# Optimization experiments

Hardware: AMD Instinct MI355X
Metric: run time of the kernel (lower is better)

Reference implementation:

```python
import jax, jax.numpy as jnp
import numpy as np

B, D_S, D_E, D_K, D_C, D_P, D_W, D_M, N_MEM, N_LEV = 2048, 1024, 1024, 256, 1024, 1024, 512, 1024, 4096, 3
SAT = 10.0


def _ln(x, scale, bias, eps=1e-6):
    mu = jnp.mean(x, axis=-1, keepdims=True)
    var = jnp.var(x, axis=-1, keepdims=True)
    return (x - mu) * jax.lax.rsqrt(var + eps) * scale + bias


def setup_inputs() -> dict:
    key = jax.random.key(0)
    ks = iter(jax.random.split(key, 48))
    rn = lambda shape, s=0.02: jax.random.normal(next(ks), shape, dtype=jnp.float32) * s
    h_q = D_S + D_E
    h_p = D_P + D_C
    return {
        "s_prev": rn((B, D_S), 1.0), "w_prev": rn((B, D_W), 1.0),
        "p_prev": rn((B, D_P), 1.0), "e_t": rn((B, D_E), 1.0),
        "M0": rn((N_MEM, D_M), 1.0), "M1": rn((N_MEM, D_M), 1.0), "M2": rn((N_MEM, D_M), 1.0),
        "K0": rn((N_MEM, D_K), 1.0), "K1": rn((N_MEM, D_K), 1.0), "K2": rn((N_MEM, D_K), 1.0),
        "Wq1": rn((h_q, h_q)), "bq1": jnp.zeros((h_q,), jnp.float32),
        "ln_q_scale": jnp.ones((h_q,), jnp.float32), "ln_q_bias": jnp.zeros((h_q,), jnp.float32),
        "Wq2": rn((h_q, D_K)), "bq2": jnp.zeros((D_K,), jnp.float32),
        "Wl0": rn((D_M, D_C)), "Wl1": rn((D_M, D_C)), "Wl2": rn((D_M, D_C)),
        "Wmix": rn((N_LEV * D_C, N_LEV)), "bmix": jnp.zeros((N_LEV,), jnp.float32),
        "Wz": rn((D_E, D_P)), "bz": jnp.zeros((D_P,), jnp.float32),
        "A_diag": jnp.zeros((D_W,), jnp.float32),
        "A_U": rn((D_W, D_W // 4), 0.01), "A_V": rn((D_W, D_W // 4), 0.01),
        "Wamod": rn((D_C, D_W)), "bamod": jnp.zeros((D_W,), jnp.float32),
        "WB": rn((D_C + D_P, D_W)), "bB": jnp.zeros((D_W,), jnp.float32),
        "Wp1": rn((h_p, h_p)), "bp1": jnp.zeros((h_p,), jnp.float32),
        "ln_p_scale": jnp.ones((h_p,), jnp.float32), "ln_p_bias": jnp.zeros((h_p,), jnp.float32),
        "Wp2": rn((h_p, D_P)), "bp2": jnp.zeros((D_P,), jnp.float32),
        "Wg": rn((D_S + D_E + D_C, D_S)), "bg": jnp.zeros((D_S,), jnp.float32),
        "U_p": rn((D_S, D_P)), "U_w": rn((D_S, D_W)),
    }


def _cell(s_prev, w_prev, p_prev, e_t, Ms, Ks, Wls,
          Wq1, bq1, ln_q_scale, ln_q_bias, Wq2, bq2, Wmix, bmix,
          Wz, bz, A_diag, A_U, A_V, Wamod, bamod, WB, bB,
          Wp1, bp1, ln_p_scale, ln_p_bias, Wp2, bp2, Wg, bg, U_p, U_w):
    # ---- CMS read: query -> per-level softmax attention -> mixed context ----
    q = jax.nn.relu(_ln(jnp.concatenate([s_prev, e_t], -1) @ Wq1 + bq1,
                        ln_q_scale, ln_q_bias)) @ Wq2 + bq2          # [B, d_k]
    scale = 1.0 / jnp.sqrt(jnp.float32(D_K))
    ctxs = []
    for M, K, Wl in zip(Ms, Ks, Wls):
        attn = jax.nn.softmax(q @ K.T * scale, axis=-1)              # [B, N]
        ctxs.append((attn @ M) @ Wl)                                 # [B, d_c]
    mix = jax.nn.softmax(jnp.concatenate(ctxs, -1) @ Wmix + bmix, axis=-1)  # [B, L]
    c_t = sum(mix[:, l:l + 1] * ctxs[l] for l in range(N_LEV))       # [B, d_c]
    # ---- HOPE core ----
    z_t = e_t @ Wz + bz                                              # [B, d_p]
    # wave: A = (diag(tanh(A_diag)*0.9) + A_U A_V^T) row-scaled by tanh(mod);
    # applied in factored form (same math, no [B,d_w,d_w] materialization)
    A_d = jnp.tanh(A_diag) * 0.9                                     # [d_w]
    mod = jnp.tanh(c_t @ Wamod + bamod)                              # [B, d_w]
    w_lin = A_d * w_prev + (w_prev @ A_V) @ A_U.T                    # A_base @ w_prev
    w_t = mod * w_lin + (jnp.concatenate([c_t, z_t], -1) @ WB + bB)  # [B, d_w]
    # particle: residual MLP
    h = jax.nn.relu(_ln(jnp.concatenate([p_prev, c_t], -1) @ Wp1 + bp1,
                        ln_p_scale, ln_p_bias))
    p_t = p_prev + h @ Wp2 + bp2                                     # [B, d_p]
    # gated fast-state mix
    g = jax.nn.sigmoid(jnp.concatenate([s_prev, e_t, c_t], -1) @ Wg + bg)
    s_t = s_prev + g * (p_t @ U_p.T) + (1.0 - g) * (w_t @ U_w.T)
    s_t = jnp.clip(s_t, -SAT, SAT)
    return s_t, w_t, p_t


def reference(s_prev, w_prev, p_prev, e_t, M0, M1, M2, K0, K1, K2,
              Wq1, bq1, ln_q_scale, ln_q_bias, Wq2, bq2,
              Wl0, Wl1, Wl2, Wmix, bmix, Wz, bz,
              A_diag, A_U, A_V, Wamod, bamod, WB, bB,
              Wp1, bp1, ln_p_scale, ln_p_bias, Wp2, bp2, Wg, bg, U_p, U_w):
    return _cell(s_prev, w_prev, p_prev, e_t, (M0, M1, M2), (K0, K1, K2), (Wl0, Wl1, Wl2),
                 Wq1, bq1, ln_q_scale, ln_q_bias, Wq2, bq2, Wmix, bmix,
                 Wz, bz, A_diag, A_U, A_V, Wamod, bamod, WB, bB,
                 Wp1, bp1, ln_p_scale, ln_p_bias, Wp2, bp2, Wg, bg, U_p, U_w)
```

## Files before the change

kernel.cpp:

```cpp
#include <hip/hip_runtime.h>

typedef __bf16 bf16x8 __attribute__((ext_vector_type(8)));
typedef __bf16 bf16x4 __attribute__((ext_vector_type(4)));
typedef float floatx4 __attribute__((ext_vector_type(4)));

__device__ __forceinline__ void gl_lds16(const __bf16* g, const __bf16* l) {
  __builtin_amdgcn_global_load_lds(
      (const __attribute__((address_space(1))) unsigned int*)g,
      (__attribute__((address_space(3))) unsigned int*)l, 16, 0, 0);
}

template <int BM, int BN>
__global__ __launch_bounds__(256)
void gemm_nt(const __bf16* __restrict__ A, const __bf16* __restrict__ Bt,
             const float* __restrict__ bias, void* __restrict__ Cv,
             int K, int lda, int ldb, int ldc, int bf16_out, float cscale,
             long sA, long sB, long sC, int nsplit)
{
  constexpr int MI = BM / 32;
  constexpr int NJ = BN / 32;
  __shared__ __align__(16) __bf16 As[BM * 32];
  __shared__ __align__(16) __bf16 Bs[BN * 32];
  const int tid = threadIdx.x;
  const int bm = blockIdx.y * BM, bn = blockIdx.x * BN;
  const int zb = blockIdx.z / nsplit, zs = blockIdx.z % nsplit;
  const __bf16* Ab = A  + (size_t)zb * sA + (size_t)zs * K;
  const __bf16* Bb = Bt + (size_t)zb * sB + (size_t)zs * K;
  const int wave = tid >> 6, lane = tid & 63;
  const int wm = (wave & 1) * (BM / 2), wn = (wave >> 1) * (BN / 2);
  const int lrow = lane & 15, quad = lane >> 4;
  const int srow = tid >> 2, scol = (tid & 3) << 3;

  const __bf16* Ap = Ab + (size_t)(bm + srow) * lda + scol;
  const __bf16* Bp = Bb + (size_t)(bn + srow) * ldb + scol;

  floatx4 acc[MI][NJ];
#pragma unroll
  for (int i = 0; i < MI; ++i)
#pragma unroll
    for (int j = 0; j < NJ; ++j) acc[i][j] = floatx4{0.f, 0.f, 0.f, 0.f};

  for (int k0 = 0; k0 < K; k0 += 32) {
#pragma unroll
    for (int r = 0; r < BM / 64; ++r)
      gl_lds16(Ap + (size_t)(64 * r) * lda + k0, &As[tid * 8 + r * 2048]);
#pragma unroll
    for (int r = 0; r < BN / 64; ++r)
      gl_lds16(Bp + (size_t)(64 * r) * ldb + k0, &Bs[tid * 8 + r * 2048]);
    __syncthreads();
    bf16x8 af[MI], bfr[NJ];
#pragma unroll
    for (int i = 0; i < MI; ++i)
      af[i] = *(const bf16x8*)&As[(wm + i * 16 + lrow) * 32 + (quad << 3)];
#pragma unroll
    for (int j = 0; j < NJ; ++j)
      bfr[j] = *(const bf16x8*)&Bs[(wn + j * 16 + lrow) * 32 + (quad << 3)];
#pragma unroll
    for (int i = 0; i < MI; ++i)
#pragma unroll
      for (int j = 0; j < NJ; ++j)
        acc[i][j] = __builtin_amdgcn_mfma_f32_16x16x32_bf16(af[i], bfr[j], acc[i][j], 0, 0, 0);
    __syncthreads();
  }

  if (bf16_out) {
    __bf16* C = (__bf16*)Cv + (size_t)blockIdx.z * sC;
#pragma unroll
    for (int i = 0; i < MI; ++i) {
      const int row0 = bm + wm + i * 16 + (quad << 2);
#pragma unroll
      for (int j = 0; j < NJ; ++j) {
        const int col = bn + wn + j * 16 + lrow;
        const float bv = bias ? bias[col] : 0.f;
#pragma unroll
        for (int r = 0; r < 4; ++r)
          C[(size_t)(row0 + r) * ldc + col] = (__bf16)((acc[i][j][r] + bv) * cscale);
      }
    }
  } else {
    float* C = (float*)Cv + (size_t)blockIdx.z * sC;
#pragma unroll
    for (int i = 0; i < MI; ++i) {
      const int row0 = bm + wm + i * 16 + (quad << 2);
#pragma unroll
      for (int j = 0; j < NJ; ++j) {
        const int col = bn + wn + j * 16 + lrow;
        const float bv = bias ? bias[col] : 0.f;
#pragma unroll
        for (int r = 0; r < 4; ++r)
          C[(size_t)(row0 + r) * ldc + col] = (acc[i][j][r] + bv) * cscale;
      }
    }
  }
}

__global__ __launch_bounds__(256)
void reduce_kernel(const __bf16* __restrict__ part, __bf16* __restrict__ out,
                   const float* __restrict__ bias, int N, int ldo, long obs,
                   long sC, int nsplit, float scale)
{
  const long idx = ((long)blockIdx.x * 256 + threadIdx.x) * 4;
  const int r = (int)(idx / N), c = (int)(idx % N);
  const __bf16* p0 = part + (size_t)blockIdx.z * nsplit * sC + idx;
  float a0 = 0.f, a1 = 0.f, a2 = 0.f, a3 = 0.f;
  for (int s = 0; s < nsplit; ++s) {
    bf16x4 v = *(const bf16x4*)(p0 + (size_t)s * sC);
    a0 += (float)v[0]; a1 += (float)v[1]; a2 += (float)v[2]; a3 += (float)v[3];
  }
  if (bias) { a0 += bias[c]; a1 += bias[c + 1]; a2 += bias[c + 2]; a3 += bias[c + 3]; }
  bf16x4 o;
  o[0] = (__bf16)(a0 * scale); o[1] = (__bf16)(a1 * scale);
  o[2] = (__bf16)(a2 * scale); o[3] = (__bf16)(a3 * scale);
  *(bf16x4*)(out + (size_t)blockIdx.z * obs + (size_t)r * ldo + c) = o;
}

struct TSegs {
  const float* src[16]; __bf16* dst[16];
  int R[16], C[16]; int prefix[17]; int nseg;
};
__global__ __launch_bounds__(256)
void tconv_batch(TSegs t)
{
  __shared__ float tile[32][33];
  int s = 0;
  while (s < t.nseg - 1 && (int)blockIdx.x >= t.prefix[s + 1]) ++s;
  const int local = blockIdx.x - t.prefix[s];
  const int Ct = t.C[s] >> 5;
  const int tr = local / Ct, tc = local - tr * Ct;
  const int r0 = tr << 5, c0 = tc << 5;
  const float* src = t.src[s];
  __bf16* dst = t.dst[s];
  const int R = t.R[s], C = t.C[s];
  const int x = threadIdx.x & 31, y = threadIdx.x >> 5;
#pragma unroll
  for (int i = 0; i < 32; i += 8)
    tile[y + i][x] = src[(size_t)(r0 + y + i) * C + c0 + x];
  __syncthreads();
#pragma unroll
  for (int i = 0; i < 32; i += 8)
    dst[(size_t)(c0 + y + i) * R + r0 + x] = (__bf16)tile[x][y + i];
}

struct FSegs {
  const float* src[16]; __bf16* dst[16];
  int rows[16], cols[16], sld[16], dld[16]; int prefix[17]; int nseg;
};
__global__ __launch_bounds__(256)
void f2b_batch(FSegs t)
{
  int s = 0;
  while (s < t.nseg - 1 && (int)blockIdx.x >= t.prefix[s + 1]) ++s;
  const long e = ((long)(blockIdx.x - t.prefix[s]) * 256 + threadIdx.x) * 4;
  const int cols = t.cols[s];
  if (e >= (long)t.rows[s] * cols) return;
  const int r = (int)(e / cols), c = (int)(e % cols);
  float4 v = *(const float4*)(t.src[s] + (size_t)r * t.sld[s] + c);
  bf16x4 o;
  o[0] = (__bf16)v.x; o[1] = (__bf16)v.y; o[2] = (__bf16)v.z; o[3] = (__bf16)v.w;
  *(bf16x4*)(t.dst[s] + (size_t)r * t.dld[s] + c) = o;
}

__global__ __launch_bounds__(256)
void ln_relu_bf16(const __bf16* __restrict__ x, const float* __restrict__ sc,
                  const float* __restrict__ bi, __bf16* __restrict__ out)
{
  const int row = blockIdx.x;
  const __bf16* xr = x + (size_t)row * 2048;
  __bf16* orow = out + (size_t)row * 2048;
  const int c = threadIdx.x << 3;
  bf16x8 v = *(const bf16x8*)&xr[c];
  float f[8], s = 0.f, ss = 0.f;
#pragma unroll
  for (int i = 0; i < 8; ++i) { f[i] = (float)v[i]; s += f[i]; ss += f[i] * f[i]; }
  __shared__ float shs[4], shss[4];
  const int lane = threadIdx.x & 63, w = threadIdx.x >> 6;
  for (int o = 32; o; o >>= 1) { s += __shfl_down(s, o, 64); ss += __shfl_down(ss, o, 64); }
  if (!lane) { shs[w] = s; shss[w] = ss; }
  __syncthreads();
  const float fs = shs[0] + shs[1] + shs[2] + shs[3];
  const float fss = shss[0] + shss[1] + shss[2] + shss[3];
  const float mu = fs * (1.f / 2048.f);
  const float rstd = rsqrtf(fss * (1.f / 2048.f) - mu * mu + 1e-6f);
  bf16x8 o;
#pragma unroll
  for (int i = 0; i < 8; ++i)
    o[i] = (__bf16)fmaxf((f[i] - mu) * rstd * sc[c + i] + bi[c + i], 0.f);
  *(bf16x8*)&orow[c] = o;
}

__global__ __launch_bounds__(256)
void softmax_bf16_kernel(__bf16* __restrict__ x)
{
  __bf16* xr = x + (size_t)blockIdx.x * 4096;
  bf16x8 v0 = *(const bf16x8*)&xr[threadIdx.x * 16];
  bf16x8 v1 = *(const bf16x8*)&xr[threadIdx.x * 16 + 8];
  float f[16];
#pragma unroll
  for (int i = 0; i < 8; ++i) { f[i] = (float)v0[i]; f[i + 8] = (float)v1[i]; }
  float m = f[0];
#pragma unroll
  for (int i = 1; i < 16; ++i) m = fmaxf(m, f[i]);
  __shared__ float sh[4];
  const int lane = threadIdx.x & 63, w = threadIdx.x >> 6;
  for (int o = 32; o; o >>= 1) m = fmaxf(m, __shfl_down(m, o, 64));
  if (!lane) sh[w] = m;
  __syncthreads();
  m = fmaxf(fmaxf(sh[0], sh[1]), fmaxf(sh[2], sh[3]));
  __syncthreads();
  float s = 0.f;
#pragma unroll
  for (int i = 0; i < 16; ++i) { f[i] = expf(f[i] - m); s += f[i]; }
  for (int o = 32; o; o >>= 1) s += __shfl_down(s, o, 64);
  if (!lane) sh[w] = s;
  __syncthreads();
  const float rs = 1.f / (sh[0] + sh[1] + sh[2] + sh[3]);
  bf16x8 o0, o1;
#pragma unroll
  for (int i = 0; i < 8; ++i) { o0[i] = (__bf16)(f[i] * rs); o1[i] = (__bf16)(f[i + 8] * rs); }
  *(bf16x8*)&xr[threadIdx.x * 16] = o0;
  *(bf16x8*)&xr[threadIdx.x * 16 + 8] = o1;
}

__global__ __launch_bounds__(256)
void wmix_kernel(const __bf16* __restrict__ ctx, const float* __restrict__ Wm,
                 const float* __restrict__ bm, float* __restrict__ mix)
{
  const int row = blockIdx.x;
  const __bf16* cr = ctx + (size_t)row * 3072;
  float a0 = 0.f, a1 = 0.f, a2 = 0.f;
  for (int c = threadIdx.x; c < 3072; c += 256) {
    float v = (float)cr[c];
    a0 = fmaf(v, Wm[c * 3 + 0], a0);
    a1 = fmaf(v, Wm[c * 3 + 1], a1);
    a2 = fmaf(v, Wm[c * 3 + 2], a2);
  }
  __shared__ float sh[3][4];
  const int lane = threadIdx.x & 63, w = threadIdx.x >> 6;
  for (int o = 32; o; o >>= 1) {
    a0 += __shfl_down(a0, o, 64); a1 += __shfl_down(a1, o, 64); a2 += __shfl_down(a2, o, 64);
  }
  if (!lane) { sh[0][w] = a0; sh[1][w] = a1; sh[2][w] = a2; }
  __syncthreads();
  if (threadIdx.x == 0) {
    float l0 = sh[0][0] + sh[0][1] + sh[0][2] + sh[0][3] + bm[0];
    float l1 = sh[1][0] + sh[1][1] + sh[1][2] + sh[1][3] + bm[1];
    float l2 = sh[2][0] + sh[2][1] + sh[2][2] + sh[2][3] + bm[2];
    float mm = fmaxf(l0, fmaxf(l1, l2));
    float e0 = expf(l0 - mm), e1 = expf(l1 - mm), e2 = expf(l2 - mm);
    float rs = 1.f / (e0 + e1 + e2);
    mix[row * 4 + 0] = e0 * rs; mix[row * 4 + 1] = e1 * rs; mix[row * 4 + 2] = e2 * rs;
  }
}

__global__ __launch_bounds__(256)
void ct_combine_kernel(const __bf16* __restrict__ ctx, const float* __restrict__ mix,
                       __bf16* __restrict__ cz, __bf16* __restrict__ pc,
                       __bf16* __restrict__ sec)
{
  const int idx = blockIdx.x * 256 + threadIdx.x;
  const int row = idx >> 10, d = idx & 1023;
  const __bf16* cr = ctx + (size_t)row * 3072 + d;
  const float v = mix[row * 4 + 0] * (float)cr[0] +
                  mix[row * 4 + 1] * (float)cr[1024] +
                  mix[row * 4 + 2] * (float)cr[2048];
  const __bf16 b = (__bf16)v;
  cz[(size_t)row * 2048 + d] = b;
  pc[(size_t)row * 2048 + 1024 + d] = b;
  sec[(size_t)row * 3072 + 2048 + d] = b;
}

__global__ __launch_bounds__(256)
void w_combine_kernel(const float* __restrict__ w_prev, const float* __restrict__ uv,
                      const float* __restrict__ amod, const float* __restrict__ wB,
                      const float* __restrict__ A_diag, float* __restrict__ w_out,
                      __bf16* __restrict__ w_bf)
{
  const int idx = blockIdx.x * 256 + threadIdx.x;
  const int d = idx & 511;
  const float Ad = tanhf(A_diag[d]) * 0.9f;
  const float wl = fmaf(Ad, w_prev[idx], uv[idx]);
  const float w = fmaf(tanhf(amod[idx]), wl, wB[idx]);
  w_out[idx] = w;
  w_bf[idx] = (__bf16)w;
}

__global__ __launch_bounds__(256)
void p_combine_kernel(const float* __restrict__ p_prev, const __bf16* __restrict__ hp,
                      float* __restrict__ p_out, __bf16* __restrict__ p_bf)
{
  const int idx = blockIdx.x * 256 + threadIdx.x;
  const float p = p_prev[idx] + (float)hp[idx];
  p_out[idx] = p;
  p_bf[idx] = (__bf16)p;
}

__global__ __launch_bounds__(256)
void s_final_kernel(const float* __restrict__ s_prev, const __bf16* __restrict__ gpre,
                    const float* __restrict__ pu, const float* __restrict__ wu,
                    float* __restrict__ s_out)
{
  const int idx = blockIdx.x * 256 + threadIdx.x;
  const float g = 1.f / (1.f + expf(-(float)gpre[idx]));
  float s = s_prev[idx] + g * pu[idx] + (1.f - g) * wu[idx];
  s = fminf(fmaxf(s, -10.f), 10.f);
  s_out[idx] = s;
}

extern "C" void kernel_launch(void* const* d_in, const int* in_sizes, int n_in,
                              void* d_out, int out_size, void* d_ws, size_t ws_size,
                              hipStream_t stream)
{
  const float* s_prev = (const float*)d_in[0];
  const float* w_prev = (const float*)d_in[1];
  const float* p_prev = (const float*)d_in[2];
  const float* e_t    = (const float*)d_in[3];
  const float* M0 = (const float*)d_in[4];
  const float* M1 = (const float*)d_in[5];
  const float* M2 = (const float*)d_in[6];
  const float* K0 = (const float*)d_in[7];
  const float* K1 = (const float*)d_in[8];
  const float* K2 = (const float*)d_in[9];
  const float* Wq1 = (const float*)d_in[10];
  const float* bq1 = (const float*)d_in[11];
  const float* lnq_s = (const float*)d_in[12];
  const float* lnq_b = (const float*)d_in[13];
  const float* Wq2 = (const float*)d_in[14];
  const float* bq2 = (const float*)d_in[15];
  const float* Wl0 = (const float*)d_in[16];
  const float* Wl1 = (const float*)d_in[17];
  const float* Wl2 = (const float*)d_in[18];
  const float* Wmix = (const float*)d_in[19];
  const float* bmix = (const float*)d_in[20];
  const float* Wz = (const float*)d_in[21];
  const float* bz = (const float*)d_in[22];
  const float* A_diag = (const float*)d_in[23];
  const float* A_U = (const float*)d_in[24];
  const float* A_V = (const float*)d_in[25];
  const float* Wamod = (const float*)d_in[26];
  const float* bamod = (const float*)d_in[27];
  const float* WB_w = (const float*)d_in[28];
  const float* bB = (const float*)d_in[29];
  const float* Wp1 = (const float*)d_in[30];
  const float* bp1 = (const float*)d_in[31];
  const float* lnp_s = (const float*)d_in[32];
  const float* lnp_b = (const float*)d_in[33];
  const float* Wp2 = (const float*)d_in[34];
  const float* bp2 = (const float*)d_in[35];
  const float* Wg = (const float*)d_in[36];
  const float* bg = (const float*)d_in[37];
  const float* U_p = (const float*)d_in[38];
  const float* U_w = (const float*)d_in[39];

  float* out_s = (float*)d_out;
  float* out_w = out_s + 2048 * 1024;
  float* out_p = out_w + 2048 * 512;

  char* base = (char*)d_ws;
  size_t off = 0;
  auto alloc = [&](size_t n) -> void* {
    void* p = base + off;
    off = (off + n + 255) & ~(size_t)255;
    return p;
  };

  __bf16* Wq1t   = (__bf16*)alloc((size_t)2048 * 2048 * 2);
  __bf16* Wq2t   = (__bf16*)alloc((size_t)256 * 2048 * 2);
  __bf16* Kb     = (__bf16*)alloc((size_t)3 * 4096 * 256 * 2);
  __bf16* Mt     = (__bf16*)alloc((size_t)3 * 1024 * 4096 * 2);
  __bf16* Wlt    = (__bf16*)alloc((size_t)3 * 1024 * 1024 * 2);
  __bf16* Wzt    = (__bf16*)alloc((size_t)1024 * 1024 * 2);
  __bf16* AVt    = (__bf16*)alloc((size_t)128 * 512 * 2);
  __bf16* AUb    = (__bf16*)alloc((size_t)512 * 128 * 2);
  __bf16* Wamodt = (__bf16*)alloc((size_t)512 * 1024 * 2);
  __bf16* WBt    = (__bf16*)alloc((size_t)512 * 2048 * 2);
  __bf16* Wp1t   = (__bf16*)alloc((size_t)2048 * 2048 * 2);
  __bf16* Wp2t   = (__bf16*)alloc((size_t)1024 * 2048 * 2);
  __bf16* Wgt    = (__bf16*)alloc((size_t)1024 * 3072 * 2);
  __bf16* Upb    = (__bf16*)alloc((size_t)1024 * 1024 * 2);
  __bf16* Uwb    = (__bf16*)alloc((size_t)1024 * 512 * 2);
  __bf16* P      = (__bf16*)alloc((size_t)6 * 2048 * 1024 * 2);
  __bf16* cat_se  = (__bf16*)alloc((size_t)2048 * 2048 * 2);
  __bf16* tmp1b   = (__bf16*)alloc((size_t)2048 * 2048 * 2);
  __bf16* hq      = (__bf16*)alloc((size_t)2048 * 2048 * 2);
  __bf16* qb      = (__bf16*)alloc((size_t)2048 * 256 * 2);
  __bf16* attn    = (__bf16*)alloc((size_t)3 * 2048 * 4096 * 2);
  __bf16* amb     = (__bf16*)alloc((size_t)3 * 2048 * 1024 * 2);
  __bf16* ctxcat  = (__bf16*)alloc((size_t)2048 * 3072 * 2);
  float*  mix     = (float*)alloc((size_t)2048 * 4 * 4);
  __bf16* cat_cz  = (__bf16*)alloc((size_t)2048 * 2048 * 2);
  __bf16* cat_pc  = (__bf16*)alloc((size_t)2048 * 2048 * 2);
  __bf16* cat_sec = (__bf16*)alloc((size_t)2048 * 3072 * 2);
  __bf16* wpb     = (__bf16*)alloc((size_t)2048 * 512 * 2);
  __bf16* uvtb    = (__bf16*)alloc((size_t)2048 * 128 * 2);
  float*  uv      = (float*)alloc((size_t)2048 * 512 * 4);
  float*  amod    = (float*)alloc((size_t)2048 * 512 * 4);
  float*  wBo     = (float*)alloc((size_t)2048 * 512 * 4);
  __bf16* wtb     = (__bf16*)alloc((size_t)2048 * 512 * 2);
  char* arec = (char*)attn;
  __bf16* hp   = (__bf16*)(arec);
  __bf16* ptb  = (__bf16*)(arec + (size_t)4  * 1024 * 1024);
  __bf16* gpre = (__bf16*)(arec + (size_t)8  * 1024 * 1024);
  float*  pu   = (float*)(arec + (size_t)12 * 1024 * 1024);
  float*  wu   = (float*)(arec + (size_t)20 * 1024 * 1024);

  auto gemm = [&](auto tag, const __bf16* Ap, const __bf16* Bp, const float* bias,
                  void* C, int M, int N, int Ksub, int lda, int ldb, int ldc,
                  int bf16o, float sc, int batch, int nsplit, long sA, long sB, long sC) {
    constexpr int BM = decltype(tag)::value >> 16, BN = decltype(tag)::value & 0xffff;
    dim3 g(N / BN, M / BM, batch * nsplit);
    gemm_nt<BM, BN><<<g, 256, 0, stream>>>(Ap, Bp, bias, C, Ksub, lda, ldb, ldc,
                                           bf16o, sc, sA, sB, sC, nsplit);
  };
  auto reduce = [&](const __bf16* part, __bf16* out, const float* bias, int M, int N,
                    int ldo, long obs, long sC, int nsplit, float sc, int batch) {
    dim3 g((unsigned)((long)M * N / 1024), 1, batch);
    reduce_kernel<<<g, 256, 0, stream>>>(part, out, bias, N, ldo, obs, sC, nsplit, sc);
  };
  using T128 = std::integral_constant<int, (128 << 16) | 128>;
  using T12864 = std::integral_constant<int, (128 << 16) | 64>;
  using T64 = std::integral_constant<int, (64 << 16) | 64>;

  {
    TSegs t{};
    const float* s[15] = {Wq1, Wq2, M0, M1, M2, Wl0, Wl1, Wl2, Wz, A_V, Wamod,
                          WB_w, Wp1, Wp2, Wg};
    __bf16* d[15] = {Wq1t, Wq2t, Mt, Mt + (size_t)1024 * 4096, Mt + (size_t)2048 * 4096,
                     Wlt, Wlt + 1024 * 1024, Wlt + 2 * 1024 * 1024, Wzt, AVt, Wamodt,
                     WBt, Wp1t, Wp2t, Wgt};
    int R[15] = {2048, 2048, 4096, 4096, 4096, 1024, 1024, 1024, 1024, 512, 1024,
                 2048, 2048, 2048, 3072};
    int C[15] = {2048, 256, 1024, 1024, 1024, 1024, 1024, 1024, 1024, 128, 512,
                 512, 2048, 1024, 1024};
    int p = 0;
    for (int i = 0; i < 15; ++i) {
      t.src[i] = s[i]; t.dst[i] = d[i]; t.R[i] = R[i]; t.C[i] = C[i];
      t.prefix[i] = p; p += (R[i] >> 5) * (C[i] >> 5);
    }
    t.prefix[15] = p; t.nseg = 15;
    tconv_batch<<<p, 256, 0, stream>>>(t);
  }
  {
    FSegs t{};
    const float* s[12] = {K0, K1, K2, A_U, U_p, U_w, s_prev, e_t, p_prev,
                          s_prev, e_t, w_prev};
    __bf16* d[12] = {Kb, Kb + 4096 * 256, Kb + 2 * 4096 * 256, AUb, Upb, Uwb,
                     cat_se, cat_se + 1024, cat_pc, cat_sec, cat_sec + 1024, wpb};
    int rows[12] = {1, 1, 1, 1, 1, 1, 2048, 2048, 2048, 2048, 2048, 1};
    int cols[12] = {4096 * 256, 4096 * 256, 4096 * 256, 512 * 128, 1024 * 1024,
                    1024 * 512, 1024, 1024, 1024, 1024, 1024, 2048 * 512};
    int sld[12] = {0, 0, 0, 0, 0, 0, 1024, 1024, 1024, 1024, 1024, 0};
    int dld[12] = {0, 0, 0, 0, 0, 0, 2048, 2048, 2048, 3072, 3072, 0};
    int p = 0;
    for (int i = 0; i < 12; ++i) {
      t.src[i] = s[i]; t.dst[i] = d[i]; t.rows[i] = rows[i]; t.cols[i] = cols[i];
      t.sld[i] = sld[i] ? sld[i] : cols[i]; t.dld[i] = dld[i] ? dld[i] : cols[i];
      t.prefix[i] = p;
      p += (int)(((long)rows[i] * cols[i] / 4 + 255) / 256);
    }
    t.prefix[12] = p; t.nseg = 12;
    f2b_batch<<<p, 256, 0, stream>>>(t);
  }

  gemm(T128{}, cat_se, Wq1t, nullptr, P, 2048, 2048, 1024, 2048, 2048, 2048, 1, 1.f,
       1, 2, 0, 0, (long)2048 * 2048);
  reduce(P, tmp1b, bq1, 2048, 2048, 2048, 0, (long)2048 * 2048, 2, 1.f, 1);
  ln_relu_bf16<<<2048, 256, 0, stream>>>(tmp1b, lnq_s, lnq_b, hq);
  gemm(T64{}, hq, Wq2t, nullptr, P, 2048, 256, 512, 2048, 2048, 256, 1, 1.f,
       1, 4, 0, 0, (long)2048 * 256);
  reduce(P, qb, bq2, 2048, 256, 256, 0, (long)2048 * 256, 4, 0.0625f, 1);

  gemm(T128{}, qb, Kb, nullptr, attn, 2048, 4096, 256, 256, 256, 4096, 1, 1.f,
       3, 1, 0, (long)4096 * 256, (long)2048 * 4096);
  softmax_bf16_kernel<<<3 * 2048, 256, 0, stream>>>(attn);
  gemm(T128{}, attn, Mt, nullptr, P, 2048, 1024, 2048, 4096, 4096, 1024, 1, 1.f,
       3, 2, (long)2048 * 4096, (long)1024 * 4096, (long)2048 * 1024);
  reduce(P, amb, nullptr, 2048, 1024, 1024, (long)2048 * 1024, (long)2048 * 1024, 2, 1.f, 3);
  gemm(T128{}, amb, Wlt, nullptr, P, 2048, 1024, 512, 1024, 1024, 1024, 1, 1.f,
       3, 2, (long)2048 * 1024, (long)1024 * 1024, (long)2048 * 1024);
  reduce(P, ctxcat, nullptr, 2048, 1024, 3072, 1024, (long)2048 * 1024, 2, 1.f, 3);
  wmix_kernel<<<2048, 256, 0, stream>>>(ctxcat, Wmix, bmix, mix);
  ct_combine_kernel<<<8192, 256, 0, stream>>>(ctxcat, mix, cat_cz, cat_pc, cat_sec);

  gemm(T12864{}, cat_se + 1024, Wzt, bz, cat_cz + 1024, 2048, 1024, 1024, 2048, 1024,
       2048, 1, 1.f, 1, 1, 0, 0, 0);
  gemm(T64{}, wpb, AVt, nullptr, uvtb, 2048, 128, 512, 512, 512, 128, 1, 1.f,
       1, 1, 0, 0, 0);
  gemm(T64{}, uvtb, AUb, nullptr, uv, 2048, 512, 128, 128, 128, 512, 0, 1.f,
       1, 1, 0, 0, 0);
  gemm(T64{}, cat_cz, Wamodt, bamod, amod, 2048, 512, 1024, 2048, 1024, 512, 0, 1.f,
       1, 1, 0, 0, 0);
  gemm(T64{}, cat_cz, WBt, bB, wBo, 2048, 512, 2048, 2048, 2048, 512, 0, 1.f,
       1, 1, 0, 0, 0);
  w_combine_kernel<<<4096, 256, 0, stream>>>(w_prev, uv, amod, wBo, A_diag, out_w, wtb);

  gemm(T128{}, cat_pc, Wp1t, nullptr, P, 2048, 2048, 1024, 2048, 2048, 2048, 1, 1.f,
       1, 2, 0, 0, (long)2048 * 2048);
  reduce(P, tmp1b, bp1, 2048, 2048, 2048, 0, (long)2048 * 2048, 2, 1.f, 1);
  ln_relu_bf16<<<2048, 256, 0, stream>>>(tmp1b, lnp_s, lnp_b, hq);
  gemm(T128{}, hq, Wp2t, nullptr, P, 2048, 1024, 512, 2048, 2048, 1024, 1, 1.f,
       1, 4, 0, 0, (long)2048 * 1024);
  reduce(P, hp, bp2, 2048, 1024, 1024, 0, (long)2048 * 1024, 4, 1.f, 1);
  p_combine_kernel<<<8192, 256, 0, stream>>>(p_prev, hp, out_p, ptb);

  gemm(T128{}, cat_sec, Wgt, nullptr, P, 2048, 1024, 768, 3072, 3072, 1024, 1, 1.f,
       1, 4, 0, 0, (long)2048 * 1024);
  reduce(P, gpre, bg, 2048, 1024, 1024, 0, (long)2048 * 1024, 4, 1.f, 1);
  gemm(T12864{}, ptb, Upb, nullptr, pu, 2048, 1024, 1024, 1024, 1024, 1024, 0, 1.f,
       1, 1, 0, 0, 0);
  gemm(T12864{}, wtb, Uwb, nullptr, wu, 2048, 1024, 512, 512, 512, 1024, 0, 1.f,
       1, 1, 0, 0, 0);
  s_final_kernel<<<8192, 256, 0, stream>>>(s_prev, gpre, pu, wu, out_s);
}
```

Before: 786.2 us.

## Fuse split-K reductions into LN/combine kernels and raise split-K factors

Split-K reductions are merged into the LayerNorm+ReLU, particle-combine and final-state kernels, which removes intermediate bf16 buffers and several launches. Split-K factors go up for many GEMMs (2→4, 1→2) to give more parallelism, and several fp32 intermediates (uv, amod, wB) are now written as bf16. The reduce kernel is widened to 8 elements per thread. In exchange there is more partial-sum traffic, a larger P buffer, and extra bf16 rounding on intermediates.

```diff
diff --git a/kernel.cpp b/kernel.cpp
--- a/kernel.cpp
+++ b/kernel.cpp
@@ -1,4 +1,5 @@
 #include <hip/hip_runtime.h>
+#include <type_traits>
 
 typedef __bf16 bf16x8 __attribute__((ext_vector_type(8)));
 typedef __bf16 bf16x4 __attribute__((ext_vector_type(4)));
@@ -99,19 +100,101 @@
                    const float* __restrict__ bias, int N, int ldo, long obs,
                    long sC, int nsplit, float scale)
 {
-  const long idx = ((long)blockIdx.x * 256 + threadIdx.x) * 4;
+  const long idx = ((long)blockIdx.x * 256 + threadIdx.x) * 8;
   const int r = (int)(idx / N), c = (int)(idx % N);
   const __bf16* p0 = part + (size_t)blockIdx.z * nsplit * sC + idx;
-  float a0 = 0.f, a1 = 0.f, a2 = 0.f, a3 = 0.f;
+  float a[8] = {0, 0, 0, 0, 0, 0, 0, 0};
   for (int s = 0; s < nsplit; ++s) {
-    bf16x4 v = *(const bf16x4*)(p0 + (size_t)s * sC);
-    a0 += (float)v[0]; a1 += (float)v[1]; a2 += (float)v[2]; a3 += (float)v[3];
-  }
-  if (bias) { a0 += bias[c]; a1 += bias[c + 1]; a2 += bias[c + 2]; a3 += bias[c + 3]; }
-  bf16x4 o;
-  o[0] = (__bf16)(a0 * scale); o[1] = (__bf16)(a1 * scale);
-  o[2] = (__bf16)(a2 * scale); o[3] = (__bf16)(a3 * scale);
-  *(bf16x4*)(out + (size_t)blockIdx.z * obs + (size_t)r * ldo + c) = o;
+    bf16x8 v = *(const bf16x8*)(p0 + (size_t)s * sC);
+#pragma unroll
+    for (int i = 0; i < 8; ++i) a[i] += (float)v[i];
+  }
+  if (bias) {
+#pragma unroll
+    for (int i = 0; i < 8; ++i) a[i] += bias[c + i];
+  }
+  bf16x8 o;
+#pragma unroll
+  for (int i = 0; i < 8; ++i) o[i] = (__bf16)(a[i] * scale);
+  *(bf16x8*)(out + (size_t)blockIdx.z * obs + (size_t)r * ldo + c) = o;
+}
+
+__global__ __launch_bounds__(256)
+void reduce_ln_relu(const __bf16* __restrict__ P, long sC, int nsplit,
+                    const float* __restrict__ bias, const float* __restrict__ sc,
+                    const float* __restrict__ bi, __bf16* __restrict__ out)
+{
+  const int row = blockIdx.x;
+  const int c = threadIdx.x << 3;
+  const __bf16* p0 = P + (size_t)row * 2048 + c;
+  float f[8] = {0, 0, 0, 0, 0, 0, 0, 0};
+  for (int s = 0; s < nsplit; ++s) {
+    bf16x8 v = *(const bf16x8*)(p0 + (size_t)s * sC);
+#pragma unroll
+    for (int i = 0; i < 8; ++i) f[i] += (float)v[i];
+  }
+  float su = 0.f, ss = 0.f;
+#pragma unroll
+  for (int i = 0; i < 8; ++i) { f[i] += bias[c + i]; su += f[i]; ss += f[i] * f[i]; }
+  __shared__ float shs[4], shss[4];
+  const int lane = threadIdx.x & 63, w = threadIdx.x >> 6;
+  for (int o = 32; o; o >>= 1) { su += __shfl_down(su, o, 64); ss += __shfl_down(ss, o, 64); }
+  if (!lane) { shs[w] = su; shss[w] = ss; }
+  __syncthreads();
+  const float fs = shs[0] + shs[1] + shs[2] + shs[3];
+  const float fss = shss[0] + shss[1] + shss[2] + shss[3];
+  const float mu = fs * (1.f / 2048.f);
+  const float rstd = rsqrtf(fss * (1.f / 2048.f) - mu * mu + 1e-6f);
+  bf16x8 o;
+#pragma unroll
+  for (int i = 0; i < 8; ++i)
+    o[i] = (__bf16)fmaxf((f[i] - mu) * rstd * sc[c + i] + bi[c + i], 0.f);
+  *(bf16x8*)&out[(size_t)row * 2048 + c] = o;
+}
+
+__global__ __launch_bounds__(256)
+void reduce_p_combine(const __bf16* __restrict__ P, long sC, int nsplit,
+                      const float* __restrict__ bp2, const float* __restrict__ p_prev,
+                      float* __restrict__ p_out, __bf16* __restrict__ p_bf)
+{
+  const long idx = ((long)blockIdx.x * 256 + threadIdx.x) * 8;
+  const int c = (int)(idx & 1023);
+  float a[8] = {0, 0, 0, 0, 0, 0, 0, 0};
+  for (int s = 0; s < nsplit; ++s) {
+    bf16x8 v = *(const bf16x8*)(P + (size_t)s * sC + idx);
+#pragma unroll
+    for (int i = 0; i < 8; ++i) a[i] += (float)v[i];
+  }
+  bf16x8 ob;
+#pragma unroll
+  for (int i = 0; i < 8; ++i) {
+    const float p = p_prev[idx + i] + a[i] + bp2[c + i];
+    p_out[idx + i] = p;
+    ob[i] = (__bf16)p;
+  }
+  *(bf16x8*)&p_bf[idx] = ob;
+}
+
+__global__ __launch_bounds__(256)
+void s_final_fused(const __bf16* __restrict__ P, long sC, int nsplit,
+                   const float* __restrict__ bg, const float* __restrict__ s_prev,
+                   const float* __restrict__ pu, const float* __restrict__ wu,
+                   float* __restrict__ s_out)
+{
+  const long idx = ((long)blockIdx.x * 256 + threadIdx.x) * 8;
+  const int c = (int)(idx & 1023);
+  float a[8] = {0, 0, 0, 0, 0, 0, 0, 0};
+  for (int s = 0; s < nsplit; ++s) {
+    bf16x8 v = *(const bf16x8*)(P + (size_t)s * sC + idx);
+#pragma unroll
+    for (int i = 0; i < 8; ++i) a[i] += (float)v[i];
+  }
+#pragma unroll
+  for (int i = 0; i < 8; ++i) {
+    const float g = 1.f / (1.f + expf(-(a[i] + bg[c + i])));
+    float s = s_prev[idx + i] + g * pu[idx + i] + (1.f - g) * wu[idx + i];
+    s_out[idx + i] = fminf(fmaxf(s, -10.f), 10.f);
+  }
 }
 
 struct TSegs {
@@ -161,34 +244,6 @@
 }
 
 __global__ __launch_bounds__(256)
-void ln_relu_bf16(const __bf16* __restrict__ x, const float* __restrict__ sc,
-                  const float* __restrict__ bi, __bf16* __restrict__ out)
-{
-  const int row = blockIdx.x;
-  const __bf16* xr = x + (size_t)row * 2048;
-  __bf16* orow = out + (size_t)row * 2048;
-  const int c = threadIdx.x << 3;
-  bf16x8 v = *(const bf16x8*)&xr[c];
-  float f[8], s = 0.f, ss = 0.f;
-#pragma unroll
-  for (int i = 0; i < 8; ++i) { f[i] = (float)v[i]; s += f[i]; ss += f[i] * f[i]; }
-  __shared__ float shs[4], shss[4];
-  const int lane = threadIdx.x & 63, w = threadIdx.x >> 6;
-  for (int o = 32; o; o >>= 1) { s += __shfl_down(s, o, 64); ss += __shfl_down(ss, o, 64); }
-  if (!lane) { shs[w] = s; shss[w] = ss; }
-  __syncthreads();
-  const float fs = shs[0] + shs[1] + shs[2] + shs[3];
-  const float fss = shss[0] + shss[1] + shss[2] + shss[3];
-  const float mu = fs * (1.f / 2048.f);
-  const float rstd = rsqrtf(fss * (1.f / 2048.f) - mu * mu + 1e-6f);
-  bf16x8 o;
-#pragma unroll
-  for (int i = 0; i < 8; ++i)
-    o[i] = (__bf16)fmaxf((f[i] - mu) * rstd * sc[c + i] + bi[c + i], 0.f);
-  *(bf16x8*)&orow[c] = o;
-}
-
-__global__ __launch_bounds__(256)
 void softmax_bf16_kernel(__bf16* __restrict__ x)
 {
   __bf16* xr = x + (size_t)blockIdx.x * 4096;
@@ -270,40 +325,18 @@
 }
 
 __global__ __launch_bounds__(256)
-void w_combine_kernel(const float* __restrict__ w_prev, const float* __restrict__ uv,
-                      const float* __restrict__ amod, const float* __restrict__ wB,
+void w_combine_kernel(const float* __restrict__ w_prev, const __bf16* __restrict__ uv,
+                      const __bf16* __restrict__ amod, const __bf16* __restrict__ wB,
                       const float* __restrict__ A_diag, float* __restrict__ w_out,
                       __bf16* __restrict__ w_bf)
 {
   const int idx = blockIdx.x * 256 + threadIdx.x;
   const int d = idx & 511;
   const float Ad = tanhf(A_diag[d]) * 0.9f;
-  const float wl = fmaf(Ad, w_prev[idx], uv[idx]);
-  const float w = fmaf(tanhf(amod[idx]), wl, wB[idx]);
+  const float wl = fmaf(Ad, w_prev[idx], (float)uv[idx]);
+  const float w = fmaf(tanhf((float)amod[idx]), wl, (float)wB[idx]);
   w_out[idx] = w;
   w_bf[idx] = (__bf16)w;
-}
-
-__global__ __launch_bounds__(256)
-void p_combine_kernel(const float* __restrict__ p_prev, const __bf16* __restrict__ hp,
-                      float* __restrict__ p_out, __bf16* __restrict__ p_bf)
-{
-  const int idx = blockIdx.x * 256 + threadIdx.x;
-  const float p = p_prev[idx] + (float)hp[idx];
-  p_out[idx] = p;
-  p_bf[idx] = (__bf16)p;
-}
-
-__global__ __launch_bounds__(256)
-void s_final_kernel(const float* __restrict__ s_prev, const __bf16* __restrict__ gpre,
-                    const float* __restrict__ pu, const float* __restrict__ wu,
-                    float* __restrict__ s_out)
-{
-  const int idx = blockIdx.x * 256 + threadIdx.x;
-  const float g = 1.f / (1.f + expf(-(float)gpre[idx]));
-  float s = s_prev[idx] + g * pu[idx] + (1.f - g) * wu[idx];
-  s = fminf(fmaxf(s, -10.f), 10.f);
-  s_out[idx] = s;
 }
 
 extern "C" void kernel_launch(void* const* d_in, const int* in_sizes, int n_in,
@@ -378,9 +411,8 @@
   __bf16* Wgt    = (__bf16*)alloc((size_t)1024 * 3072 * 2);
   __bf16* Upb    = (__bf16*)alloc((size_t)1024 * 1024 * 2);
   __bf16* Uwb    = (__bf16*)alloc((size_t)1024 * 512 * 2);
-  __bf16* P      = (__bf16*)alloc((size_t)6 * 2048 * 1024 * 2);
+  __bf16* P      = (__bf16*)alloc((size_t)12 * 2048 * 1024 * 2);
   __bf16* cat_se  = (__bf16*)alloc((size_t)2048 * 2048 * 2);
-  __bf16* tmp1b   = (__bf16*)alloc((size_t)2048 * 2048 * 2);
   __bf16* hq      = (__bf16*)alloc((size_t)2048 * 2048 * 2);
   __bf16* qb      = (__bf16*)alloc((size_t)2048 * 256 * 2);
   __bf16* attn    = (__bf16*)alloc((size_t)3 * 2048 * 4096 * 2);
@@ -392,16 +424,14 @@
   __bf16* cat_sec = (__bf16*)alloc((size_t)2048 * 3072 * 2);
   __bf16* wpb     = (__bf16*)alloc((size_t)2048 * 512 * 2);
   __bf16* uvtb    = (__bf16*)alloc((size_t)2048 * 128 * 2);
-  float*  uv      = (float*)alloc((size_t)2048 * 512 * 4);
-  float*  amod    = (float*)alloc((size_t)2048 * 512 * 4);
-  float*  wBo     = (float*)alloc((size_t)2048 * 512 * 4);
+  __bf16* uv      = (__bf16*)alloc((size_t)2048 * 512 * 2);
+  __bf16* amod    = (__bf16*)alloc((size_t)2048 * 512 * 2);
+  __bf16* wBo     = (__bf16*)alloc((size_t)2048 * 512 * 2);
   __bf16* wtb     = (__bf16*)alloc((size_t)2048 * 512 * 2);
   char* arec = (char*)attn;
-  __bf16* hp   = (__bf16*)(arec);
-  __bf16* ptb  = (__bf16*)(arec + (size_t)4  * 1024 * 1024);
-  __bf16* gpre = (__bf16*)(arec + (size_t)8  * 1024 * 1024);
-  float*  pu   = (float*)(arec + (size_t)12 * 1024 * 1024);
-  float*  wu   = (float*)(arec + (size_t)20 * 1024 * 1024);
+  __bf16* ptb = (__bf16*)(arec);
+  float*  pu  = (float*)(arec + (size_t)4  * 1024 * 1024);
+  float*  wu  = (float*)(arec + (size_t)12 * 1024 * 1024);
 
   auto gemm = [&](auto tag, const __bf16* Ap, const __bf16* Bp, const float* bias,
                   void* C, int M, int N, int Ksub, int lda, int ldb, int ldc,
@@ -413,12 +443,16 @@
   };
   auto reduce = [&](const __bf16* part, __bf16* out, const float* bias, int M, int N,
                     int ldo, long obs, long sC, int nsplit, float sc, int batch) {
-    dim3 g((unsigned)((long)M * N / 1024), 1, batch);
+    dim3 g((unsigned)((long)M * N / 2048), 1, batch);
     reduce_kernel<<<g, 256, 0, stream>>>(part, out, bias, N, ldo, obs, sC, nsplit, sc);
   };
   using T128 = std::integral_constant<int, (128 << 16) | 128>;
   using T12864 = std::integral_constant<int, (128 << 16) | 64>;
   using T64 = std::integral_constant<int, (64 << 16) | 64>;
+  const long S21 = (long)2048 * 1024;
+  const long S22 = (long)2048 * 2048;
+  const long S25 = (long)2048 * 512;
+  const long S2q = (long)2048 * 256;
 
   {
     TSegs t{};
@@ -461,53 +495,53 @@
     f2b_batch<<<p, 256, 0, stream>>>(t);
   }
 
-  gemm(T128{}, cat_se, Wq1t, nullptr, P, 2048, 2048, 1024, 2048, 2048, 2048, 1, 1.f,
-       1, 2, 0, 0, (long)2048 * 2048);
-  reduce(P, tmp1b, bq1, 2048, 2048, 2048, 0, (long)2048 * 2048, 2, 1.f, 1);
-  ln_relu_bf16<<<2048, 256, 0, stream>>>(tmp1b, lnq_s, lnq_b, hq);
+  gemm(T128{}, cat_se, Wq1t, nullptr, P, 2048, 2048, 512, 2048, 2048, 2048, 1, 1.f,
+       1, 4, 0, 0, S22);
+  reduce_ln_relu<<<2048, 256, 0, stream>>>(P, S22, 4, bq1, lnq_s, lnq_b, hq);
   gemm(T64{}, hq, Wq2t, nullptr, P, 2048, 256, 512, 2048, 2048, 256, 1, 1.f,
-       1, 4, 0, 0, (long)2048 * 256);
-  reduce(P, qb, bq2, 2048, 256, 256, 0, (long)2048 * 256, 4, 0.0625f, 1);
+       1, 4, 0, 0, S2q);
+  reduce(P, qb, bq2, 2048, 256, 256, 0, S2q, 4, 0.0625f, 1);
 
   gemm(T128{}, qb, Kb, nullptr, attn, 2048, 4096, 256, 256, 256, 4096, 1, 1.f,
        3, 1, 0, (long)4096 * 256, (long)2048 * 4096);
   softmax_bf16_kernel<<<3 * 2048, 256, 0, stream>>>(attn);
-  gemm(T128{}, attn, Mt, nullptr, P, 2048, 1024, 2048, 4096, 4096, 1024, 1, 1.f,
-       3, 2, (long)2048 * 4096, (long)1024 * 4096, (long)2048 * 1024);
-  reduce(P, amb, nullptr, 2048, 1024, 1024, (long)2048 * 1024, (long)2048 * 1024, 2, 1.f, 3);
-  gemm(T128{}, amb, Wlt, nullptr, P, 2048, 1024, 512, 1024, 1024, 1024, 1, 1.f,
-       3, 2, (long)2048 * 1024, (long)1024 * 1024, (long)2048 * 1024);
-  reduce(P, ctxcat, nullptr, 2048, 1024, 3072, 1024, (long)2048 * 1024, 2, 1.f, 3);
+  gemm(T128{}, attn, Mt, nullptr, P, 2048, 1024, 1024, 4096, 4096, 1024, 1, 1.f,
+       3, 4, (long)2048 * 4096, (long)1024 * 4096, S21);
+  reduce(P, amb, nullptr, 2048, 1024, 1024, S21, S21, 4, 1.f, 3);
+  gemm(T128{}, amb, Wlt, nullptr, P, 2048, 1024, 256, 1024, 1024, 1024, 1, 1.f,
+       3, 4, S21, (long)1024 * 1024, S21);
+  reduce(P, ctxcat, nullptr, 2048, 1024, 3072, 1024, S21, 4, 1.f, 3);
   wmix_kernel<<<2048, 256, 0, stream>>>(ctxcat, Wmix, bmix, mix);
   ct_combine_kernel<<<8192, 256, 0, stream>>>(ctxcat, mix, cat_cz, cat_pc, cat_sec);
 
-  gemm(T12864{}, cat_se + 1024, Wzt, bz, cat_cz + 1024, 2048, 1024, 1024, 2048, 1024,
-       2048, 1, 1.f, 1, 1, 0, 0, 0);
-  gemm(T64{}, wpb, AVt, nullptr, uvtb, 2048, 128, 512, 512, 512, 128, 1, 1.f,
+  gemm(T12864{}, cat_se + 1024, Wzt, nullptr, P, 2048, 1024, 512, 2048, 1024,
+       1024, 1, 1.f, 1, 2, 0, 0, S21);
+  reduce(P, cat_cz + 1024, bz, 2048, 1024, 2048, 0, S21, 2, 1.f, 1);
+  gemm(T64{}, wpb, AVt, nullptr, P, 2048, 128, 128, 512, 512, 128, 1, 1.f,
+       1, 4, 0, 0, (long)2048 * 128);
+  reduce(P, uvtb, nullptr, 2048, 128, 128, 0, (long)2048 * 128, 4, 1.f, 1);
+  gemm(T64{}, uvtb, AUb, nullptr, uv, 2048, 512, 128, 128, 128, 512, 1, 1.f,
        1, 1, 0, 0, 0);
-  gemm(T64{}, uvtb, AUb, nullptr, uv, 2048, 512, 128, 128, 128, 512, 0, 1.f,
-       1, 1, 0, 0, 0);
-  gemm(T64{}, cat_cz, Wamodt, bamod, amod, 2048, 512, 1024, 2048, 1024, 512, 0, 1.f,
-       1, 1, 0, 0, 0);
-  gemm(T64{}, cat_cz, WBt, bB, wBo, 2048, 512, 2048, 2048, 2048, 512, 0, 1.f,
-       1, 1, 0, 0, 0);
+  gemm(T64{}, cat_cz, Wamodt, nullptr, P, 2048, 512, 512, 2048, 1024, 512, 1, 1.f,
+       1, 2, 0, 0, S25);
+  reduce(P, amod, bamod, 2048, 512, 512, 0, S25, 2, 1.f, 1);
+  gemm(T64{}, cat_cz, WBt, nullptr, P + 2 * S25, 2048, 512, 1024, 2048, 2048, 512, 1, 1.f,
+       1, 2, 0, 0, S25);
+  reduce(P + 2 * S25, wBo, bB, 2048, 512, 512, 0, S25, 2, 1.f, 1);
   w_combine_kernel<<<4096, 256, 0, stream>>>(w_prev, uv, amod, wBo, A_diag, out_w, wtb);
 
-  gemm(T128{}, cat_pc, Wp1t, nullptr, P, 2048, 2048, 1024, 2048, 2048, 2048, 1, 1.f,
-       1, 2, 0, 0, (long)2048 * 2048);
-  reduce(P, tmp1b, bp1, 2048, 2048, 2048, 0, (long)2048 * 2048, 2, 1.f, 1);
-  ln_relu_bf16<<<2048, 256, 0, stream>>>(tmp1b, lnp_s, lnp_b, hq);
+  gemm(T128{}, cat_pc, Wp1t, nullptr, P, 2048, 2048, 512, 2048, 2048, 2048, 1, 1.f,
+       1, 4, 0, 0, S22);
+  reduce_ln_relu<<<2048, 256, 0, stream>>>(P, S22, 4, bp1, lnp_s, lnp_b, hq);
   gemm(T128{}, hq, Wp2t, nullptr, P, 2048, 1024, 512, 2048, 2048, 1024, 1, 1.f,
-       1, 4, 0, 0, (long)2048 * 1024);
-  reduce(P, hp, bp2, 2048, 1024, 1024, 0, (long)2048 * 1024, 4, 1.f, 1);
-  p_combine_kernel<<<8192, 256, 0, stream>>>(p_prev, hp, out_p, ptb);
-
-  gemm(T128{}, cat_sec, Wgt, nullptr, P, 2048, 1024, 768, 3072, 3072, 1024, 1, 1.f,
-       1, 4, 0, 0, (long)2048 * 1024);
-  reduce(P, gpre, bg, 2048, 1024, 1024, 0, (long)2048 * 1024, 4, 1.f, 1);
+       1, 4, 0, 0, S21);
+  reduce_p_combine<<<1024, 256, 0, stream>>>(P, S21, 4, bp2, p_prev, out_p, ptb);
+
+  gemm(T12864{}, cat_sec, Wgt, nullptr, P, 2048, 1024, 768, 3072, 3072, 1024, 1, 1.f,
+       1, 4, 0, 0, S21);
   gemm(T12864{}, ptb, Upb, nullptr, pu, 2048, 1024, 1024, 1024, 1024, 1024, 0, 1.f,
        1, 1, 0, 0, 0);
   gemm(T12864{}, wtb, Uwb, nullptr, wu, 2048, 1024, 512, 512, 512, 1024, 0, 1.f,
        1, 1, 0, 0, 0);
-  s_final_kernel<<<8192, 256, 0, stream>>>(s_prev, gpre, pu, wu, out_s);
-}
+  s_final_fused<<<1024, 256, 0, stream>>>(P, S21, 4, bg, s_prev, pu, wu, out_s);
+}
```

Result: no change. 786.6 us (+0.1%).
